# Performance work log

Measured on AMD Instinct MI355X. Metric: run time of the kernel, lower is better.

Reference implementation:

```python
import jax, jax.numpy as jnp
import numpy as np

DIM = 1024
HEADS = 16
HEAD_DIM = DIM // HEADS
SCALE = HEAD_DIM ** -0.5


def setup_inputs() -> dict:
    key = jax.random.key(0)
    ks = jax.random.split(key, 9)
    b, n, m = 4, 1024, 1024
    x = jax.random.normal(ks[0], (b, n, DIM), dtype=jnp.float32)
    context = jax.random.normal(ks[1], (b, m, DIM), dtype=jnp.float32)
    mask = jax.random.randint(ks[2], (b, n, 32, 32), 0, 2, dtype=jnp.int32)
    s = DIM ** -0.5
    Wq = jax.random.normal(ks[3], (DIM, DIM), dtype=jnp.float32) * s
    bq = jnp.zeros((DIM,), dtype=jnp.float32)
    Wkv = jax.random.normal(ks[4], (DIM, 2 * DIM), dtype=jnp.float32) * s
    bkv = jnp.zeros((2 * DIM,), dtype=jnp.float32)
    Wp = jax.random.normal(ks[5], (DIM, DIM), dtype=jnp.float32) * s
    bp = jnp.zeros((DIM,), dtype=jnp.float32)
    return {"x": x, "context": context, "mask": mask,
            "Wq": Wq, "bq": bq, "Wkv": Wkv, "bkv": bkv, "Wp": Wp, "bp": bp}


def reference(x, context, mask, Wq, bq, Wkv, bkv, Wp, bp):
    b, n, _ = x.shape
    m = context.shape[1]
    h, d = HEADS, HEAD_DIM
    # projections
    q = (x @ Wq + bq).reshape(b, n, h, d).transpose(0, 2, 1, 3)       # [b,h,n,d]
    kv = (context @ Wkv + bkv).reshape(b, m, 2, h, d)
    k = kv[:, :, 0].transpose(0, 2, 1, 3)                              # [b,h,m,d]
    v = kv[:, :, 1].transpose(0, 2, 1, 3)                              # [b,h,m,d]
    dots = jnp.einsum('bhnd,bhmd->bhnm', q, k) * SCALE                 # [b,h,n,m]
    # mask: [b,n,H,W] -> [b,1,n,m]; masked_fill where mask == 0
    mflat = mask.reshape(b, n, m)[:, None]                             # [b,1,n,m]
    dots = jnp.where(mflat == 0, -jnp.inf, dots)
    attn = jax.nn.softmax(dots, axis=-1)
    out = jnp.einsum('bhnm,bhmd->bhnd', attn, v)
    out = out.transpose(0, 2, 1, 3).reshape(b, n, h * d)
    return out @ Wp + bp
```

## Files before the change

### kernel.cpp

```cpp
#include <hip/hip_runtime.h>

typedef __bf16 bf16;
typedef __bf16 bf16x8 __attribute__((ext_vector_type(8)));
typedef __bf16 bf16x4 __attribute__((ext_vector_type(4)));
typedef float f32x4 __attribute__((ext_vector_type(4)));
typedef unsigned long long u64;

#define MFMA16(a, b, c) __builtin_amdgcn_mfma_f32_16x16x32_bf16(a, b, c, 0, 0, 0)

__device__ __forceinline__ void gl_lds16(const void* g, void* l) {
  __builtin_amdgcn_global_load_lds(
      (const __attribute__((address_space(1))) unsigned int*)g,
      (__attribute__((address_space(3))) unsigned int*)l, 16, 0, 0);
}

template <int N>
__device__ __forceinline__ void wait_vmcnt() {
  asm volatile("s_waitcnt vmcnt(%0)" ::"n"(N) : "memory");
}

__device__ __forceinline__ void bar() {
  asm volatile("" ::: "memory");
  __builtin_amdgcn_s_barrier();
  asm volatile("" ::: "memory");
}

__global__ __launch_bounds__(256)
void prep_k(const float* __restrict__ Wq, const float* __restrict__ Wkv,
            const float* __restrict__ Wp, const int* __restrict__ mask,
            const float* __restrict__ context, const float* __restrict__ x,
            bf16* __restrict__ BqkvT, bf16* __restrict__ WpT,
            u64* __restrict__ maskbits, bf16* __restrict__ cb,
            bf16* __restrict__ xb) {
  const int bx = blockIdx.x;
  const int tid = threadIdx.x;
  if (bx >= 3328) {
    const size_t i = ((size_t)(bx - 3328) * 256 + tid) * 8;
    f32x4 a0 = *(const f32x4*)(x + i);
    f32x4 a1 = *(const f32x4*)(x + i + 4);
    bf16x8 t;
#pragma unroll
    for (int j = 0; j < 4; ++j) { t[j] = (bf16)a0[j]; t[4 + j] = (bf16)a1[j]; }
    *(bf16x8*)(xb + i) = t;
    return;
  }
  if (bx >= 1280) {
    const size_t i = ((size_t)(bx - 1280) * 256 + tid) * 8;
    f32x4 a0 = *(const f32x4*)(context + i);
    f32x4 a1 = *(const f32x4*)(context + i + 4);
    bf16x8 t;
#pragma unroll
    for (int j = 0; j < 4; ++j) { t[j] = (bf16)a0[j]; t[4 + j] = (bf16)a1[j]; }
    *(bf16x8*)(cb + i) = t;
    return;
  }
  if (bx >= 1024) {
    const int idx = (bx - 1024) * 256 + tid;
    const int4* p = (const int4*)(mask + (size_t)idx * 64);
    u64 v = 0;
#pragma unroll
    for (int i = 0; i < 16; ++i) {
      int4 m = p[i];
      v |= (u64)(m.x != 0) << (4 * i);
      v |= (u64)(m.y != 0) << (4 * i + 1);
      v |= (u64)(m.z != 0) << (4 * i + 2);
      v |= (u64)(m.w != 0) << (4 * i + 3);
    }
    maskbits[idx] = v;
    return;
  }
  const int ct = bx >> 4, rt = bx & 15;
  const float* src;
  bf16* dst;
  int C, c0, drow0;
  if (ct < 16) {
    src = Wq; C = 1024; c0 = ct * 64; dst = BqkvT; drow0 = c0;
  } else if (ct < 48) {
    src = Wkv; C = 2048; c0 = (ct - 16) * 64; dst = BqkvT; drow0 = 1024 + c0;
  } else {
    src = Wp; C = 1024; c0 = (ct - 48) * 64; dst = WpT; drow0 = c0;
  }
  __shared__ bf16 T[64][72];
  const int r0 = rt * 64;
#pragma unroll
  for (int i = 0; i < 2; ++i) {
    int c = i * 256 + tid;
    int row = c >> 3, col = (c & 7) * 8;
    const float* sp = &src[(size_t)(r0 + row) * C + c0 + col];
    f32x4 a0 = *(const f32x4*)sp;
    f32x4 a1 = *(const f32x4*)(sp + 4);
    bf16x8 t;
#pragma unroll
    for (int j = 0; j < 4; ++j) { t[j] = (bf16)a0[j]; t[4 + j] = (bf16)a1[j]; }
    *(bf16x8*)&T[row][col] = t;
  }
  __syncthreads();
#pragma unroll
  for (int i = 0; i < 2; ++i) {
    int c = i * 256 + tid;
    int orow = c >> 3, ocol = (c & 7) * 8;
    bf16x8 v;
#pragma unroll
    for (int j = 0; j < 8; ++j) v[j] = T[ocol + j][orow];
    *(bf16x8*)&dst[(size_t)(drow0 + orow) * 1024 + r0 + ocol] = v;
  }
}

template <int EPI, int BN>
__global__ __launch_bounds__(256, BN == 128 ? 3 : 4)
void gemm_p3(const bf16* __restrict__ A0, const bf16* __restrict__ A1,
             const bf16* __restrict__ Bt, const float* __restrict__ bias0,
             const float* __restrict__ bias1, bf16* __restrict__ oq,
             bf16* __restrict__ ok, bf16* __restrict__ ovt,
             float* __restrict__ outf) {
  constexpr int NJ = BN / 32;
  constexpr int S = 2 + BN / 64;
  __shared__ bf16 As[3][128][32];
  __shared__ bf16 Bs[3][BN][32];
  const int tid = threadIdx.x;
  const int lane = tid & 63;
  const int w = tid >> 6;
  const int wm = (w >> 1) * 64;
  const int wn = (w & 1) * (BN / 2);
  const int l15 = lane & 15, l4 = lane >> 4;
  const int lrow = lane >> 2;
  const int lcg = (lane & 3) ^ ((lrow >> 1) & 3);
  const int rdc = (l4 ^ ((l15 >> 1) & 3)) * 8;
  const int m0 = blockIdx.x * 128;
  const int n0 = blockIdx.y * BN;

  const bf16* Asrc = (EPI == 1) ? ((n0 < 1024) ? A0 : A1) : A0;

  float bc[NJ];
#pragma unroll
  for (int j = 0; j < NJ; ++j) {
    const int col = n0 + wn + j * 16 + l15;
    if (EPI == 1) bc[j] = (col < 1024) ? bias0[col] : bias1[col - 1024];
    else bc[j] = bias0[col];
  }

  f32x4 acc[4][NJ] = {};

#define STAGE(kk, buf)                                                        \
  {                                                                           \
    _Pragma("unroll") for (int it = 0; it < 2; ++it) {                        \
      const int r = w * 32 + it * 16;                                         \
      gl_lds16(&Asrc[(size_t)(m0 + r + lrow) * 1024 + (kk) + lcg * 8],        \
               &As[buf][r][0]);                                               \
    }                                                                         \
    _Pragma("unroll") for (int it = 0; it < BN / 64; ++it) {                  \
      const int r = w * (BN / 4) + it * 16;                                   \
      gl_lds16(&Bt[(size_t)(n0 + r + lrow) * 1024 + (kk) + lcg * 8],          \
               &Bs[buf][r][0]);                                               \
    }                                                                         \
  }

#define COMPUTE(buf)                                                          \
  {                                                                           \
    bf16x8 af[4], bfr[NJ];                                                    \
    _Pragma("unroll") for (int i = 0; i < 4; ++i) af[i] =                     \
        *(const bf16x8*)&As[buf][wm + i * 16 + l15][rdc];                     \
    _Pragma("unroll") for (int j = 0; j < NJ; ++j) bfr[j] =                   \
        *(const bf16x8*)&Bs[buf][wn + j * 16 + l15][rdc];                     \
    _Pragma("unroll") for (int i = 0; i < 4; ++i)                             \
        _Pragma("unroll") for (int j = 0; j < NJ; ++j) acc[i][j] =            \
            MFMA16(af[i], bfr[j], acc[i][j]);                                 \
  }

  STAGE(0, 0);
  STAGE(32, 1);
#pragma unroll 3
  for (int k = 0; k < 30; ++k) {
    wait_vmcnt<S>();
    bar();
    STAGE((k + 2) * 32, (k + 2) % 3);
    COMPUTE(k % 3);
  }
  wait_vmcnt<S>();
  bar();
  COMPUTE(0);
  wait_vmcnt<0>();
  bar();
  COMPUTE(1);
#undef STAGE
#undef COMPUTE

  const float SCALE2 = 0.18033688011112042f;
#pragma unroll
  for (int j = 0; j < NJ; ++j) {
    const int col = n0 + wn + j * 16 + l15;
#pragma unroll
    for (int i = 0; i < 4; ++i) {
#pragma unroll
      for (int r = 0; r < 4; ++r) {
        const int row = m0 + wm + i * 16 + l4 * 4 + r;
        const float v = acc[i][j][r] + bc[j];
        if (EPI == 0) {
          outf[(size_t)row * 1024 + col] = v;
        } else {
          const int b = row >> 10, n = row & 1023;
          if (col < 1024) {
            const int h = col >> 6, d = col & 63;
            oq[(((size_t)(b * 16 + h)) * 1024 + n) * 64 + d] =
                (bf16)(v * SCALE2);
          } else {
            const int ckv = col - 1024;
            const int s = ckv >> 10, c2 = ckv & 1023;
            const int h = c2 >> 6, d = c2 & 63;
            if (s == 0)
              ok[(((size_t)(b * 16 + h)) * 1024 + n) * 64 + d] = (bf16)v;
            else
              ovt[(((size_t)(b * 16 + h)) * 64 + d) * 1024 + n] = (bf16)v;
          }
        }
      }
    }
  }
}

__global__ __launch_bounds__(256, 4)
void attn_kernel(const bf16* __restrict__ q, const bf16* __restrict__ k,
                 const bf16* __restrict__ vT, const u64* __restrict__ maskbits,
                 bf16* __restrict__ ao) {
  const int bh = blockIdx.x;
  const int ntile = blockIdx.y;
  const int b = bh >> 4, h = bh & 15;
  const int tid = threadIdx.x;
  const int lane = tid & 63;
  const int w = tid >> 6;
  const int l15 = lane & 15, l4 = lane >> 4;

  __shared__ bf16 Ks[2][64][64];
  __shared__ bf16 Vts[2][64][64];
  __shared__ bf16 Pw[4][16][64];

  const size_t base = (size_t)bh * 65536;
  const int nrow0 = ntile * 64 + w * 16;

  bf16x8 qf[2];
#pragma unroll
  for (int ks = 0; ks < 2; ++ks)
    qf[ks] = *(const bf16x8*)&q[base + (size_t)(nrow0 + l15) * 64 + ks * 32 +
                                l4 * 8];

  const u64* mb = maskbits + (size_t)(b * 1024 + nrow0 + l15) * 16;

  const int srow = lane >> 3;
  const int sgl = (lane & 7) ^ srow;
  const bf16* kp = &k[base + (size_t)(w * 16 + srow) * 64 + sgl * 8];
  const bf16* vp = &vT[base + (size_t)(w * 16 + srow) * 1024 + sgl * 8];

  const int rc0 = ((0 + l4) ^ (l15 & 7)) * 8;
  const int rc1 = ((4 + l4) ^ (l15 & 7)) * 8;

  f32x4 o[4] = {};
  float lsum = 0.0f;

#define STAGEA(mt_, buf_)                                                     \
  {                                                                           \
    _Pragma("unroll") for (int it = 0; it < 2; ++it) {                        \
      gl_lds16(kp + (size_t)((mt_)*64 + it * 8) * 64,                         \
               &Ks[buf_][w * 16 + it * 8][0]);                                \
      gl_lds16(vp + (size_t)(it * 8) * 1024 + (mt_)*64,                       \
               &Vts[buf_][w * 16 + it * 8][0]);                               \
    }                                                                         \
  }

  STAGEA(0, 0);
  for (int mt = 0; mt < 16; ++mt) {
    const int cur = mt & 1;
    __syncthreads();
    if (mt < 15) STAGEA(mt + 1, cur ^ 1);
    const u64 wmt = mb[mt];

    f32x4 s[4];
#pragma unroll
    for (int sub = 0; sub < 4; ++sub)
      s[sub] = f32x4{-12.f, -12.f, -12.f, -12.f};
    __builtin_amdgcn_s_setprio(1);
#pragma unroll
    for (int sub = 0; sub < 4; ++sub) {
      bf16x8 kf0 = *(const bf16x8*)&Ks[cur][sub * 16 + l15][rc0];
      bf16x8 kf1 = *(const bf16x8*)&Ks[cur][sub * 16 + l15][rc1];
      s[sub] = MFMA16(kf0, qf[0], s[sub]);
      s[sub] = MFMA16(kf1, qf[1], s[sub]);
    }
    __builtin_amdgcn_s_setprio(0);

#pragma unroll
    for (int sub = 0; sub < 4; ++sub) {
      const int kbit = sub * 16 + l4 * 4;
      float p[4];
#pragma unroll
      for (int r = 0; r < 4; ++r) {
        float e = exp2f(s[sub][r]);
        p[r] = ((wmt >> (kbit + r)) & 1) ? e : 0.0f;
      }
      lsum += (p[0] + p[1]) + (p[2] + p[3]);
      bf16x4 pv;
#pragma unroll
      for (int r = 0; r < 4; ++r) pv[r] = (bf16)p[r];
      const int gw = sub * 2 + (l4 >> 1);
      char* pd = (char*)&Pw[w][l15][0] + ((gw ^ (l15 & 7)) * 16 + (l4 & 1) * 8);
      *(bf16x4*)pd = pv;
    }

    bf16x8 af0 = *(const bf16x8*)&Pw[w][l15][rc0];
    bf16x8 af1 = *(const bf16x8*)&Pw[w][l15][rc1];
    __builtin_amdgcn_s_setprio(1);
#pragma unroll
    for (int sub = 0; sub < 4; ++sub) {
      bf16x8 vf0 = *(const bf16x8*)&Vts[cur][sub * 16 + l15][rc0];
      bf16x8 vf1 = *(const bf16x8*)&Vts[cur][sub * 16 + l15][rc1];
      o[sub] = MFMA16(af0, vf0, o[sub]);
      o[sub] = MFMA16(af1, vf1, o[sub]);
    }
    __builtin_amdgcn_s_setprio(0);
  }
#undef STAGEA

  float t = lsum;
  t += __shfl_xor(t, 16);
  t += __shfl_xor(t, 32);
  float inv[4];
#pragma unroll
  for (int r = 0; r < 4; ++r) inv[r] = 1.0f / __shfl(t, l4 * 4 + r);

#pragma unroll
  for (int sub = 0; sub < 4; ++sub) {
#pragma unroll
    for (int r = 0; r < 4; ++r) {
      const int n = nrow0 + l4 * 4 + r;
      const size_t idx =
          ((size_t)(b * 1024 + n)) * 1024 + h * 64 + sub * 16 + l15;
      ao[idx] = (bf16)(o[sub][r] * inv[r]);
    }
  }
}

extern "C" void kernel_launch(void* const* d_in, const int* in_sizes, int n_in,
                              void* d_out, int out_size, void* d_ws,
                              size_t ws_size, hipStream_t stream) {
  const float* x = (const float*)d_in[0];
  const float* context = (const float*)d_in[1];
  const int* mask = (const int*)d_in[2];
  const float* Wq = (const float*)d_in[3];
  const float* bq = (const float*)d_in[4];
  const float* Wkv = (const float*)d_in[5];
  const float* bkv = (const float*)d_in[6];
  const float* Wp = (const float*)d_in[7];
  const float* bp = (const float*)d_in[8];
  float* out = (float*)d_out;

  char* ws = (char*)d_ws;
  bf16* cb = (bf16*)(ws);
  bf16* aow = (bf16*)(ws);
  bf16* xb = (bf16*)(ws + (8ull << 20));
  bf16* BqkvT = (bf16*)(ws + (16ull << 20));
  bf16* qw = (bf16*)(ws + (22ull << 20));
  bf16* kw = (bf16*)(ws + (30ull << 20));
  bf16* vtw = (bf16*)(ws + (38ull << 20));
  u64* maskbits = (u64*)(ws + (46ull << 20));
  bf16* WpT = (bf16*)(ws + (46ull << 20) + (512ull << 10));

  const dim3 blk(256);

  prep_k<<<dim3(5376), blk, 0, stream>>>(Wq, Wkv, Wp, mask, context, x, BqkvT,
                                         WpT, maskbits, cb, xb);

  gemm_p3<1, 128><<<dim3(32, 24), blk, 0, stream>>>(xb, cb, BqkvT, bq, bkv,
                                                    qw, kw, vtw, nullptr);

  attn_kernel<<<dim3(64, 16), blk, 0, stream>>>(qw, kw, vtw, maskbits, aow);

  gemm_p3<0, 64><<<dim3(32, 16), blk, 0, stream>>>(aow, nullptr, WpT, bp,
                                                   nullptr, nullptr, nullptr,
                                                   nullptr, out);
}
```

Baseline: 209.3 us.

## Fuse fp32-to-bf16 activation conversion into QKV projection GEMM

Drops the separate conversion of x and context to bf16 in the prep kernel. A new QKV GEMM kernel reads fp32 activations directly into registers, converts them and writes them to swizzled LDS, while the weights are still staged with global_load_lds in a double-buffered loop. This saves the write and re-read of two 8 MB bf16 intermediates. In exchange the A tile is loaded with fp32 global loads, which doubles its bytes, adds register pressure and conversion work inside the main loop, and the pipeline drops from three stages to two.

Result: slower. 223.3 us (+6.7%).

```diff
diff --git a/kernel.cpp b/kernel.cpp
--- a/kernel.cpp
+++ b/kernel.cpp
@@ -28,32 +28,10 @@
 __global__ __launch_bounds__(256)
 void prep_k(const float* __restrict__ Wq, const float* __restrict__ Wkv,
             const float* __restrict__ Wp, const int* __restrict__ mask,
-            const float* __restrict__ context, const float* __restrict__ x,
             bf16* __restrict__ BqkvT, bf16* __restrict__ WpT,
-            u64* __restrict__ maskbits, bf16* __restrict__ cb,
-            bf16* __restrict__ xb) {
+            u64* __restrict__ maskbits) {
   const int bx = blockIdx.x;
   const int tid = threadIdx.x;
-  if (bx >= 3328) {
-    const size_t i = ((size_t)(bx - 3328) * 256 + tid) * 8;
-    f32x4 a0 = *(const f32x4*)(x + i);
-    f32x4 a1 = *(const f32x4*)(x + i + 4);
-    bf16x8 t;
-#pragma unroll
-    for (int j = 0; j < 4; ++j) { t[j] = (bf16)a0[j]; t[4 + j] = (bf16)a1[j]; }
-    *(bf16x8*)(xb + i) = t;
-    return;
-  }
-  if (bx >= 1280) {
-    const size_t i = ((size_t)(bx - 1280) * 256 + tid) * 8;
-    f32x4 a0 = *(const f32x4*)(context + i);
-    f32x4 a1 = *(const f32x4*)(context + i + 4);
-    bf16x8 t;
-#pragma unroll
-    for (int j = 0; j < 4; ++j) { t[j] = (bf16)a0[j]; t[4 + j] = (bf16)a1[j]; }
-    *(bf16x8*)(cb + i) = t;
-    return;
-  }
   if (bx >= 1024) {
     const int idx = (bx - 1024) * 256 + tid;
     const int4* p = (const int4*)(mask + (size_t)idx * 64);
@@ -103,6 +81,138 @@
 #pragma unroll
     for (int j = 0; j < 8; ++j) v[j] = T[ocol + j][orow];
     *(bf16x8*)&dst[(size_t)(drow0 + orow) * 1024 + r0 + ocol] = v;
+  }
+}
+
+__global__ __launch_bounds__(256, 3)
+void gemm_qkv(const float* __restrict__ x, const float* __restrict__ ctx,
+              const bf16* __restrict__ Bt, const float* __restrict__ bq,
+              const float* __restrict__ bkv, bf16* __restrict__ oq,
+              bf16* __restrict__ ok, bf16* __restrict__ ovt) {
+  __shared__ bf16 As[2][128][32];
+  __shared__ bf16 Bs[2][128][32];
+  const int tid = threadIdx.x;
+  const int lane = tid & 63;
+  const int w = tid >> 6;
+  const int wm = (w >> 1) * 64;
+  const int wn = (w & 1) * 64;
+  const int l15 = lane & 15, l4 = lane >> 4;
+  const int lrow = lane >> 2;
+  const int lcg = (lane & 3) ^ ((lrow >> 1) & 3);
+  const int rdc = (l4 ^ ((l15 >> 1) & 3)) * 8;
+  const int ar = tid >> 1;
+  const int ag = (tid & 1) * 2;
+  const int asw = (ar >> 1) & 3;
+  const int m0 = blockIdx.x * 128;
+  const int n0 = blockIdx.y * 128;
+
+  const float* Af = (n0 < 1024) ? x : ctx;
+
+  float bc[4];
+#pragma unroll
+  for (int j = 0; j < 4; ++j) {
+    const int col = n0 + wn + j * 16 + l15;
+    bc[j] = (col < 1024) ? bq[col] : bkv[col - 1024];
+  }
+
+  f32x4 acc[4][4] = {};
+  f32x4 pf[4];
+  bf16x8 cfA[4], cfB[4], nfA[4], nfB[4];
+
+#define LOADA(kk)                                                             \
+  {                                                                           \
+    const float* ap = &Af[(size_t)(m0 + ar) * 1024 + (kk) + ag * 8];          \
+    pf[0] = *(const f32x4*)ap;                                                \
+    pf[1] = *(const f32x4*)(ap + 4);                                          \
+    pf[2] = *(const f32x4*)(ap + 8);                                          \
+    pf[3] = *(const f32x4*)(ap + 12);                                         \
+  }
+#define COMMITA(buf)                                                          \
+  {                                                                           \
+    bf16x8 t0, t1;                                                            \
+    _Pragma("unroll") for (int u = 0; u < 4; ++u) {                           \
+      t0[u] = (bf16)pf[0][u]; t0[4 + u] = (bf16)pf[1][u];                     \
+      t1[u] = (bf16)pf[2][u]; t1[4 + u] = (bf16)pf[3][u];                     \
+    }                                                                         \
+    *(bf16x8*)&As[buf][ar][(ag ^ asw) * 8] = t0;                              \
+    *(bf16x8*)&As[buf][ar][((ag + 1) ^ asw) * 8] = t1;                        \
+  }
+#define STAGEB(kk, buf)                                                       \
+  _Pragma("unroll") for (int it = 0; it < 2; ++it) {                          \
+    const int r = w * 32 + it * 16;                                           \
+    gl_lds16(&Bt[(size_t)(n0 + r + lrow) * 1024 + (kk) + lcg * 8],            \
+             &Bs[buf][r][0]);                                                 \
+  }
+#define LOADFRAG(dA, dB, buf)                                                 \
+  {                                                                           \
+    _Pragma("unroll") for (int i = 0; i < 4; ++i) dA[i] =                     \
+        *(const bf16x8*)&As[buf][wm + i * 16 + l15][rdc];                     \
+    _Pragma("unroll") for (int j = 0; j < 4; ++j) dB[j] =                     \
+        *(const bf16x8*)&Bs[buf][wn + j * 16 + l15][rdc];                     \
+  }
+#define MFMA_BLK(fA, fB)                                                      \
+  _Pragma("unroll") for (int i = 0; i < 4; ++i)                               \
+      _Pragma("unroll") for (int j = 0; j < 4; ++j) acc[i][j] =               \
+          MFMA16(fA[i], fB[j], acc[i][j]);
+
+  LOADA(0);
+  STAGEB(0, 0);
+  COMMITA(0);
+  __syncthreads();
+  LOADA(32);
+  STAGEB(32, 1);
+  LOADFRAG(cfA, cfB, 0);
+  COMMITA(1);
+
+  for (int t = 0; t < 30; t += 2) {
+    __syncthreads();
+    LOADA((t + 2) * 32);
+    STAGEB((t + 2) * 32, 0);
+    LOADFRAG(nfA, nfB, 1);
+    MFMA_BLK(cfA, cfB);
+    COMMITA(0);
+    __syncthreads();
+    LOADA((t + 3) * 32);
+    STAGEB((t + 3) * 32, 1);
+    LOADFRAG(cfA, cfB, 0);
+    MFMA_BLK(nfA, nfB);
+    COMMITA(1);
+  }
+  __syncthreads();
+  LOADFRAG(nfA, nfB, 1);
+  MFMA_BLK(cfA, cfB);
+  MFMA_BLK(nfA, nfB);
+#undef LOADA
+#undef COMMITA
+#undef STAGEB
+#undef LOADFRAG
+#undef MFMA_BLK
+
+  const float SCALE2 = 0.18033688011112042f;
+#pragma unroll
+  for (int j = 0; j < 4; ++j) {
+    const int col = n0 + wn + j * 16 + l15;
+#pragma unroll
+    for (int i = 0; i < 4; ++i) {
+#pragma unroll
+      for (int r = 0; r < 4; ++r) {
+        const int row = m0 + wm + i * 16 + l4 * 4 + r;
+        const float v = acc[i][j][r] + bc[j];
+        const int b = row >> 10, n = row & 1023;
+        if (col < 1024) {
+          const int h = col >> 6, d = col & 63;
+          oq[(((size_t)(b * 16 + h)) * 1024 + n) * 64 + d] = (bf16)(v * SCALE2);
+        } else {
+          const int ckv = col - 1024;
+          const int s = ckv >> 10, c2 = ckv & 1023;
+          const int h = c2 >> 6, d = c2 & 63;
+          if (s == 0)
+            ok[(((size_t)(b * 16 + h)) * 1024 + n) * 64 + d] = (bf16)v;
+          else
+            ovt[(((size_t)(b * 16 + h)) * 64 + d) * 1024 + n] = (bf16)v;
+        }
+      }
+    }
   }
 }
 
@@ -353,23 +463,21 @@
   float* out = (float*)d_out;
 
   char* ws = (char*)d_ws;
-  bf16* cb = (bf16*)(ws);
   bf16* aow = (bf16*)(ws);
-  bf16* xb = (bf16*)(ws + (8ull << 20));
-  bf16* BqkvT = (bf16*)(ws + (16ull << 20));
-  bf16* qw = (bf16*)(ws + (22ull << 20));
-  bf16* kw = (bf16*)(ws + (30ull << 20));
-  bf16* vtw = (bf16*)(ws + (38ull << 20));
-  u64* maskbits = (u64*)(ws + (46ull << 20));
-  bf16* WpT = (bf16*)(ws + (46ull << 20) + (512ull << 10));
+  bf16* BqkvT = (bf16*)(ws + (8ull << 20));
+  bf16* qw = (bf16*)(ws + (14ull << 20));
+  bf16* kw = (bf16*)(ws + (22ull << 20));
+  bf16* vtw = (bf16*)(ws + (30ull << 20));
+  u64* maskbits = (u64*)(ws + (38ull << 20));
+  bf16* WpT = (bf16*)(ws + (38ull << 20) + (512ull << 10));
 
   const dim3 blk(256);
 
-  prep_k<<<dim3(5376), blk, 0, stream>>>(Wq, Wkv, Wp, mask, context, x, BqkvT,
-                                         WpT, maskbits, cb, xb);
-
-  gemm_p3<1, 128><<<dim3(32, 24), blk, 0, stream>>>(xb, cb, BqkvT, bq, bkv,
-                                                    qw, kw, vtw, nullptr);
+  prep_k<<<dim3(1280), blk, 0, stream>>>(Wq, Wkv, Wp, mask, BqkvT, WpT,
+                                         maskbits);
+
+  gemm_qkv<<<dim3(32, 24), blk, 0, stream>>>(x, context, BqkvT, bq, bkv, qw,
+                                             kw, vtw);
 
   attn_kernel<<<dim3(64, 16), blk, 0, stream>>>(qw, kw, vtw, maskbits, aow);
 
```

## Double query rows per attention wave and add double-buffered QKV GEMM variant

Applied to the files above, without the earlier changes.

The attention kernel now gives each wave 32 query rows instead of 16, so every K/V tile loaded into LDS serves twice as many MFMAs. The grid shrinks to 8 query tiles per head and launch bounds drop to 2 blocks per SM. The QKV projection switches to a new two-stage double-buffered GEMM that replaces the triple-buffered one. The trade-off is more registers and fewer resident waves per CU in exchange for less LDS staging and fewer barriers per MFMA.

After: 212.9 us. About the same (+1.7%).

```diff
diff --git a/kernel.cpp b/kernel.cpp
--- a/kernel.cpp
+++ b/kernel.cpp
@@ -103,6 +103,106 @@
 #pragma unroll
     for (int j = 0; j < 8; ++j) v[j] = T[ocol + j][orow];
     *(bf16x8*)&dst[(size_t)(drow0 + orow) * 1024 + r0 + ocol] = v;
+  }
+}
+
+template <int EPI, int BN>
+__global__ __launch_bounds__(256, 3)
+void gemm_db2(const bf16* __restrict__ A0, const bf16* __restrict__ A1,
+              const bf16* __restrict__ Bt, const float* __restrict__ bias0,
+              const float* __restrict__ bias1, bf16* __restrict__ oq,
+              bf16* __restrict__ ok, bf16* __restrict__ ovt,
+              float* __restrict__ outf) {
+  constexpr int NJ = BN / 32;
+  __shared__ bf16 As[2][128][32];
+  __shared__ bf16 Bs[2][BN][32];
+  const int tid = threadIdx.x;
+  const int lane = tid & 63;
+  const int w = tid >> 6;
+  const int wm = (w >> 1) * 64;
+  const int wn = (w & 1) * (BN / 2);
+  const int l15 = lane & 15, l4 = lane >> 4;
+  const int lrow = lane >> 2;
+  const int lcg = (lane & 3) ^ ((lrow >> 1) & 3);
+  const int rdc = (l4 ^ ((l15 >> 1) & 3)) * 8;
+  const int m0 = blockIdx.x * 128;
+  const int n0 = blockIdx.y * BN;
+
+  const bf16* Asrc = (EPI == 1) ? ((n0 < 1024) ? A0 : A1) : A0;
+
+  f32x4 acc[4][NJ] = {};
+
+#define STAGE(kk, buf)                                                        \
+  {                                                                           \
+    _Pragma("unroll") for (int it = 0; it < 2; ++it) {                        \
+      const int r = w * 32 + it * 16;                                         \
+      gl_lds16(&Asrc[(size_t)(m0 + r + lrow) * 1024 + (kk) + lcg * 8],        \
+               &As[buf][r][0]);                                               \
+    }                                                                         \
+    _Pragma("unroll") for (int it = 0; it < BN / 64; ++it) {                  \
+      const int r = w * (BN / 4) + it * 16;                                   \
+      gl_lds16(&Bt[(size_t)(n0 + r + lrow) * 1024 + (kk) + lcg * 8],          \
+               &Bs[buf][r][0]);                                               \
+    }                                                                         \
+  }
+
+#define COMPUTE(buf)                                                          \
+  {                                                                           \
+    bf16x8 af[4], bfr[NJ];                                                    \
+    _Pragma("unroll") for (int i = 0; i < 4; ++i) af[i] =                     \
+        *(const bf16x8*)&As[buf][wm + i * 16 + l15][rdc];                     \
+    _Pragma("unroll") for (int j = 0; j < NJ; ++j) bfr[j] =                   \
+        *(const bf16x8*)&Bs[buf][wn + j * 16 + l15][rdc];                     \
+    _Pragma("unroll") for (int i = 0; i < 4; ++i)                             \
+        _Pragma("unroll") for (int j = 0; j < NJ; ++j) acc[i][j] =            \
+            MFMA16(af[i], bfr[j], acc[i][j]);                                 \
+  }
+
+  STAGE(0, 0);
+  for (int k = 0; k < 32; k += 2) {
+    __syncthreads();
+    STAGE((k + 1) * 32, 1);
+    COMPUTE(0);
+    __syncthreads();
+    if (k < 30) STAGE((k + 2) * 32, 0);
+    COMPUTE(1);
+  }
+#undef STAGE
+#undef COMPUTE
+
+  const float SCALE2 = 0.18033688011112042f;
+#pragma unroll
+  for (int j = 0; j < NJ; ++j) {
+    const int col = n0 + wn + j * 16 + l15;
+    float bc;
+    if (EPI == 1) bc = (col < 1024) ? bias0[col] : bias1[col - 1024];
+    else bc = bias0[col];
+#pragma unroll
+    for (int i = 0; i < 4; ++i) {
+#pragma unroll
+      for (int r = 0; r < 4; ++r) {
+        const int row = m0 + wm + i * 16 + l4 * 4 + r;
+        const float v = acc[i][j][r] + bc;
+        if (EPI == 0) {
+          outf[(size_t)row * 1024 + col] = v;
+        } else {
+          const int b = row >> 10, n = row & 1023;
+          if (col < 1024) {
+            const int h = col >> 6, d = col & 63;
+            oq[(((size_t)(b * 16 + h)) * 1024 + n) * 64 + d] =
+                (bf16)(v * SCALE2);
+          } else {
+            const int ckv = col - 1024;
+            const int s = ckv >> 10, c2 = ckv & 1023;
+            const int h = c2 >> 6, d = c2 & 63;
+            if (s == 0)
+              ok[(((size_t)(b * 16 + h)) * 1024 + n) * 64 + d] = (bf16)v;
+            else
+              ovt[(((size_t)(b * 16 + h)) * 64 + d) * 1024 + n] = (bf16)v;
+          }
+        }
+      }
+    }
   }
 }
 
@@ -218,7 +318,7 @@
   }
 }
 
-__global__ __launch_bounds__(256, 4)
+__global__ __launch_bounds__(256, 2)
 void attn_kernel(const bf16* __restrict__ q, const bf16* __restrict__ k,
                  const bf16* __restrict__ vT, const u64* __restrict__ maskbits,
                  bf16* __restrict__ ao) {
@@ -232,16 +332,19 @@
 
   __shared__ bf16 Ks[2][64][64];
   __shared__ bf16 Vts[2][64][64];
-  __shared__ bf16 Pw[4][16][64];
+  __shared__ bf16 Pw[4][32][64];
 
   const size_t base = (size_t)bh * 65536;
-  const int nrow0 = ntile * 64 + w * 16;
-
-  bf16x8 qf[2];
-#pragma unroll
-  for (int ks = 0; ks < 2; ++ks)
-    qf[ks] = *(const bf16x8*)&q[base + (size_t)(nrow0 + l15) * 64 + ks * 32 +
-                                l4 * 8];
+  const int nrow0 = ntile * 128 + w * 32;
+
+  bf16x8 qf[2][2];
+#pragma unroll
+  for (int f = 0; f < 2; ++f)
+#pragma unroll
+    for (int ks = 0; ks < 2; ++ks)
+      qf[f][ks] = *(const bf16x8*)&q[base +
+                                     (size_t)(nrow0 + f * 16 + l15) * 64 +
+                                     ks * 32 + l4 * 8];
 
   const u64* mb = maskbits + (size_t)(b * 1024 + nrow0 + l15) * 16;
 
@@ -253,8 +356,8 @@
   const int rc0 = ((0 + l4) ^ (l15 & 7)) * 8;
   const int rc1 = ((4 + l4) ^ (l15 & 7)) * 8;
 
-  f32x4 o[4] = {};
-  float lsum = 0.0f;
+  f32x4 o[2][4] = {};
+  float lsum[2] = {0.0f, 0.0f};
 
 #define STAGEA(mt_, buf_)                                                     \
   {                                                                           \
@@ -271,69 +374,91 @@
     const int cur = mt & 1;
     __syncthreads();
     if (mt < 15) STAGEA(mt + 1, cur ^ 1);
-    const u64 wmt = mb[mt];
-
-    f32x4 s[4];
-#pragma unroll
-    for (int sub = 0; sub < 4; ++sub)
-      s[sub] = f32x4{-12.f, -12.f, -12.f, -12.f};
+    const u64 wm0 = mb[mt];
+    const u64 wm1 = mb[256 + mt];
+
+    f32x4 s[2][4];
+#pragma unroll
+    for (int f = 0; f < 2; ++f)
+#pragma unroll
+      for (int sub = 0; sub < 4; ++sub)
+        s[f][sub] = f32x4{-12.f, -12.f, -12.f, -12.f};
     __builtin_amdgcn_s_setprio(1);
 #pragma unroll
     for (int sub = 0; sub < 4; ++sub) {
       bf16x8 kf0 = *(const bf16x8*)&Ks[cur][sub * 16 + l15][rc0];
       bf16x8 kf1 = *(const bf16x8*)&Ks[cur][sub * 16 + l15][rc1];
-      s[sub] = MFMA16(kf0, qf[0], s[sub]);
-      s[sub] = MFMA16(kf1, qf[1], s[sub]);
+      s[0][sub] = MFMA16(kf0, qf[0][0], s[0][sub]);
+      s[0][sub] = MFMA16(kf1, qf[0][1], s[0][sub]);
+      s[1][sub] = MFMA16(kf0, qf[1][0], s[1][sub]);
+      s[1][sub] = MFMA16(kf1, qf[1][1], s[1][sub]);
     }
     __builtin_amdgcn_s_setprio(0);
 
 #pragma unroll
-    for (int sub = 0; sub < 4; ++sub) {
-      const int kbit = sub * 16 + l4 * 4;
-      float p[4];
-#pragma unroll
-      for (int r = 0; r < 4; ++r) {
-        float e = exp2f(s[sub][r]);
-        p[r] = ((wmt >> (kbit + r)) & 1) ? e : 0.0f;
+    for (int f = 0; f < 2; ++f) {
+      const u64 wmt = f ? wm1 : wm0;
+#pragma unroll
+      for (int sub = 0; sub < 4; ++sub) {
+        const int kbit = sub * 16 + l4 * 4;
+        float p[4];
+#pragma unroll
+        for (int r = 0; r < 4; ++r) {
+          float e = exp2f(s[f][sub][r]);
+          p[r] = ((wmt >> (kbit + r)) & 1) ? e : 0.0f;
+        }
+        lsum[f] += (p[0] + p[1]) + (p[2] + p[3]);
+        bf16x4 pv;
+#pragma unroll
+        for (int r = 0; r < 4; ++r) pv[r] = (bf16)p[r];
+        const int gw = sub * 2 + (l4 >> 1);
+        char* pd = (char*)&Pw[w][f * 16 + l15][0] +
+                   ((gw ^ (l15 & 7)) * 16 + (l4 & 1) * 8);
+        *(bf16x4*)pd = pv;
       }
-      lsum += (p[0] + p[1]) + (p[2] + p[3]);
-      bf16x4 pv;
-#pragma unroll
-      for (int r = 0; r < 4; ++r) pv[r] = (bf16)p[r];
-      const int gw = sub * 2 + (l4 >> 1);
-      char* pd = (char*)&Pw[w][l15][0] + ((gw ^ (l15 & 7)) * 16 + (l4 & 1) * 8);
-      *(bf16x4*)pd = pv;
-    }
-
-    bf16x8 af0 = *(const bf16x8*)&Pw[w][l15][rc0];
-    bf16x8 af1 = *(const bf16x8*)&Pw[w][l15][rc1];
+    }
+
+    bf16x8 af[2][2];
+#pragma unroll
+    for (int f = 0; f < 2; ++f) {
+      af[f][0] = *(const bf16x8*)&Pw[w][f * 16 + l15][rc0];
+      af[f][1] = *(const bf16x8*)&Pw[w][f * 16 + l15][rc1];
+    }
     __builtin_amdgcn_s_setprio(1);
 #pragma unroll
     for (int sub = 0; sub < 4; ++sub) {
       bf16x8 vf0 = *(const bf16x8*)&Vts[cur][sub * 16 + l15][rc0];
       bf16x8 vf1 = *(const bf16x8*)&Vts[cur][sub * 16 + l15][rc1];
-      o[sub] = MFMA16(af0, vf0, o[sub]);
-      o[sub] = MFMA16(af1, vf1, o[sub]);
+      o[0][sub] = MFMA16(af[0][0], vf0, o[0][sub]);
+      o[0][sub] = MFMA16(af[0][1], vf1, o[0][sub]);
+      o[1][sub] = MFMA16(af[1][0], vf0, o[1][sub]);
+      o[1][sub] = MFMA16(af[1][1], vf1, o[1][sub]);
     }
     __builtin_amdgcn_s_setprio(0);
   }
 #undef STAGEA
 
-  float t = lsum;
-  t += __shfl_xor(t, 16);
-  t += __shfl_xor(t, 32);
-  float inv[4];
-#pragma unroll
-  for (int r = 0; r < 4; ++r) inv[r] = 1.0f / __shfl(t, l4 * 4 + r);
-
-#pragma unroll
-  for (int sub = 0; sub < 4; ++sub) {
-#pragma unroll
-    for (int r = 0; r < 4; ++r) {
-      const int n = nrow0 + l4 * 4 + r;
-      const size_t idx =
-          ((size_t)(b * 1024 + n)) * 1024 + h * 64 + sub * 16 + l15;
-      ao[idx] = (bf16)(o[sub][r] * inv[r]);
+  float inv[2][4];
+#pragma unroll
+  for (int f = 0; f < 2; ++f) {
+    float t = lsum[f];
+    t += __shfl_xor(t, 16);
+    t += __shfl_xor(t, 32);
+#pragma unroll
+    for (int r = 0; r < 4; ++r) inv[f][r] = 1.0f / __shfl(t, l4 * 4 + r);
+  }
+
+#pragma unroll
+  for (int f = 0; f < 2; ++f) {
+#pragma unroll
+    for (int sub = 0; sub < 4; ++sub) {
+#pragma unroll
+      for (int r = 0; r < 4; ++r) {
+        const int n = nrow0 + f * 16 + l4 * 4 + r;
+        const size_t idx =
+            ((size_t)(b * 1024 + n)) * 1024 + h * 64 + sub * 16 + l15;
+        ao[idx] = (bf16)(o[f][sub][r] * inv[f][r]);
+      }
     }
   }
 }
@@ -368,10 +493,10 @@
   prep_k<<<dim3(5376), blk, 0, stream>>>(Wq, Wkv, Wp, mask, context, x, BqkvT,
                                          WpT, maskbits, cb, xb);
 
-  gemm_p3<1, 128><<<dim3(32, 24), blk, 0, stream>>>(xb, cb, BqkvT, bq, bkv,
-                                                    qw, kw, vtw, nullptr);
-
-  attn_kernel<<<dim3(64, 16), blk, 0, stream>>>(qw, kw, vtw, maskbits, aow);
+  gemm_db2<1, 128><<<dim3(32, 24), blk, 0, stream>>>(xb, cb, BqkvT, bq, bkv,
+                                                     qw, kw, vtw, nullptr);
+
+  attn_kernel<<<dim3(64, 8), blk, 0, stream>>>(qw, kw, vtw, maskbits, aow);
 
   gemm_p3<0, 64><<<dim3(32, 16), blk, 0, stream>>>(aow, nullptr, WpT, bp,
                                                    nullptr, nullptr, nullptr,
```

## Process 32 query rows per warp in attention to reuse K/V tiles

Applied to the files above, without the earlier changes.

Each attention warp now computes two 16-row query fragments against the same K and V tiles in LDS, so each block covers 128 query rows and the grid is halved. This doubles the MFMA work per LDS load of K/V and halves total K/V staging traffic. Mask words for the next tile are prefetched one iteration early. The cost is more registers (launch bounds lowered to 2 blocks) and fewer blocks in flight, which may leave CUs underused.

Result: slower. 214.1 us (+2.3%).

```diff
diff --git a/kernel.cpp b/kernel.cpp
--- a/kernel.cpp
+++ b/kernel.cpp
@@ -218,7 +218,7 @@
   }
 }
 
-__global__ __launch_bounds__(256, 4)
+__global__ __launch_bounds__(256, 2)
 void attn_kernel(const bf16* __restrict__ q, const bf16* __restrict__ k,
                  const bf16* __restrict__ vT, const u64* __restrict__ maskbits,
                  bf16* __restrict__ ao) {
@@ -232,16 +232,19 @@
 
   __shared__ bf16 Ks[2][64][64];
   __shared__ bf16 Vts[2][64][64];
-  __shared__ bf16 Pw[4][16][64];
+  __shared__ bf16 Pw[4][32][64];
 
   const size_t base = (size_t)bh * 65536;
-  const int nrow0 = ntile * 64 + w * 16;
-
-  bf16x8 qf[2];
-#pragma unroll
-  for (int ks = 0; ks < 2; ++ks)
-    qf[ks] = *(const bf16x8*)&q[base + (size_t)(nrow0 + l15) * 64 + ks * 32 +
-                                l4 * 8];
+  const int nrow0 = ntile * 128 + w * 32;
+
+  bf16x8 qf[2][2];
+#pragma unroll
+  for (int f = 0; f < 2; ++f)
+#pragma unroll
+    for (int ks = 0; ks < 2; ++ks)
+      qf[f][ks] = *(const bf16x8*)&q[base +
+                                     (size_t)(nrow0 + f * 16 + l15) * 64 +
+                                     ks * 32 + l4 * 8];
 
   const u64* mb = maskbits + (size_t)(b * 1024 + nrow0 + l15) * 16;
 
@@ -253,8 +256,8 @@
   const int rc0 = ((0 + l4) ^ (l15 & 7)) * 8;
   const int rc1 = ((4 + l4) ^ (l15 & 7)) * 8;
 
-  f32x4 o[4] = {};
-  float lsum = 0.0f;
+  f32x4 o[2][4] = {};
+  float lsum[2] = {0.0f, 0.0f};
 
 #define STAGEA(mt_, buf_)                                                     \
   {                                                                           \
@@ -267,73 +270,103 @@
   }
 
   STAGEA(0, 0);
+  u64 wm0 = mb[0];
+  u64 wm1 = mb[256];
   for (int mt = 0; mt < 16; ++mt) {
     const int cur = mt & 1;
     __syncthreads();
     if (mt < 15) STAGEA(mt + 1, cur ^ 1);
-    const u64 wmt = mb[mt];
-
-    f32x4 s[4];
-#pragma unroll
-    for (int sub = 0; sub < 4; ++sub)
-      s[sub] = f32x4{-12.f, -12.f, -12.f, -12.f};
+    u64 nm0 = 0, nm1 = 0;
+    if (mt < 15) {
+      nm0 = mb[mt + 1];
+      nm1 = mb[256 + mt + 1];
+    }
+
+    f32x4 s[2][4];
+#pragma unroll
+    for (int f = 0; f < 2; ++f)
+#pragma unroll
+      for (int sub = 0; sub < 4; ++sub)
+        s[f][sub] = f32x4{-12.f, -12.f, -12.f, -12.f};
     __builtin_amdgcn_s_setprio(1);
 #pragma unroll
     for (int sub = 0; sub < 4; ++sub) {
       bf16x8 kf0 = *(const bf16x8*)&Ks[cur][sub * 16 + l15][rc0];
       bf16x8 kf1 = *(const bf16x8*)&Ks[cur][sub * 16 + l15][rc1];
-      s[sub] = MFMA16(kf0, qf[0], s[sub]);
-      s[sub] = MFMA16(kf1, qf[1], s[sub]);
+      s[0][sub] = MFMA16(kf0, qf[0][0], s[0][sub]);
+      s[0][sub] = MFMA16(kf1, qf[0][1], s[0][sub]);
+      s[1][sub] = MFMA16(kf0, qf[1][0], s[1][sub]);
+      s[1][sub] = MFMA16(kf1, qf[1][1], s[1][sub]);
     }
     __builtin_amdgcn_s_setprio(0);
 
 #pragma unroll
-    for (int sub = 0; sub < 4; ++sub) {
-      const int kbit = sub * 16 + l4 * 4;
-      float p[4];
-#pragma unroll
-      for (int r = 0; r < 4; ++r) {
-        float e = exp2f(s[sub][r]);
-        p[r] = ((wmt >> (kbit + r)) & 1) ? e : 0.0f;
+    for (int f = 0; f < 2; ++f) {
+      const u64 wmt = f ? wm1 : wm0;
+#pragma unroll
+      for (int sub = 0; sub < 4; ++sub) {
+        const int kbit = sub * 16 + l4 * 4;
+        float p[4];
+#pragma unroll
+        for (int r = 0; r < 4; ++r) {
+          float e = exp2f(s[f][sub][r]);
+          p[r] = ((wmt >> (kbit + r)) & 1) ? e : 0.0f;
+        }
+        lsum[f] += (p[0] + p[1]) + (p[2] + p[3]);
+        bf16x4 pv;
+#pragma unroll
+        for (int r = 0; r < 4; ++r) pv[r] = (bf16)p[r];
+        const int gw = sub * 2 + (l4 >> 1);
+        char* pd = (char*)&Pw[w][f * 16 + l15][0] +
+                   ((gw ^ (l15 & 7)) * 16 + (l4 & 1) * 8);
+        *(bf16x4*)pd = pv;
       }
-      lsum += (p[0] + p[1]) + (p[2] + p[3]);
-      bf16x4 pv;
-#pragma unroll
-      for (int r = 0; r < 4; ++r) pv[r] = (bf16)p[r];
-      const int gw = sub * 2 + (l4 >> 1);
-      char* pd = (char*)&Pw[w][l15][0] + ((gw ^ (l15 & 7)) * 16 + (l4 & 1) * 8);
-      *(bf16x4*)pd = pv;
-    }
-
-    bf16x8 af0 = *(const bf16x8*)&Pw[w][l15][rc0];
-    bf16x8 af1 = *(const bf16x8*)&Pw[w][l15][rc1];
+    }
+
+    bf16x8 af[2][2];
+#pragma unroll
+    for (int f = 0; f < 2; ++f) {
+      af[f][0] = *(const bf16x8*)&Pw[w][f * 16 + l15][rc0];
+      af[f][1] = *(const bf16x8*)&Pw[w][f * 16 + l15][rc1];
+    }
     __builtin_amdgcn_s_setprio(1);
 #pragma unroll
     for (int sub = 0; sub < 4; ++sub) {
       bf16x8 vf0 = *(const bf16x8*)&Vts[cur][sub * 16 + l15][rc0];
       bf16x8 vf1 = *(const bf16x8*)&Vts[cur][sub * 16 + l15][rc1];
-      o[sub] = MFMA16(af0, vf0, o[sub]);
-      o[sub] = MFMA16(af1, vf1, o[sub]);
+      o[0][sub] = MFMA16(af[0][0], vf0, o[0][sub]);
+      o[0][sub] = MFMA16(af[0][1], vf1, o[0][sub]);
+      o[1][sub] = MFMA16(af[1][0], vf0, o[1][sub]);
+      o[1][sub] = MFMA16(af[1][1], vf1, o[1][sub]);
     }
     __builtin_amdgcn_s_setprio(0);
+
+    wm0 = nm0;
+    wm1 = nm1;
   }
 #undef STAGEA
 
-  float t = lsum;
-  t += __shfl_xor(t, 16);
-  t += __shfl_xor(t, 32);
-  float inv[4];
-#pragma unroll
-  for (int r = 0; r < 4; ++r) inv[r] = 1.0f / __shfl(t, l4 * 4 + r);
-
-#pragma unroll
-  for (int sub = 0; sub < 4; ++sub) {
-#pragma unroll
-    for (int r = 0; r < 4; ++r) {
-      const int n = nrow0 + l4 * 4 + r;
-      const size_t idx =
-          ((size_t)(b * 1024 + n)) * 1024 + h * 64 + sub * 16 + l15;
-      ao[idx] = (bf16)(o[sub][r] * inv[r]);
+  float inv[2][4];
+#pragma unroll
+  for (int f = 0; f < 2; ++f) {
+    float t = lsum[f];
+    t += __shfl_xor(t, 16);
+    t += __shfl_xor(t, 32);
+#pragma unroll
+    for (int r = 0; r < 4; ++r) inv[f][r] = 1.0f / __shfl(t, l4 * 4 + r);
+  }
+
+#pragma unroll
+  for (int f = 0; f < 2; ++f) {
+#pragma unroll
+    for (int sub = 0; sub < 4; ++sub) {
+#pragma unroll
+      for (int r = 0; r < 4; ++r) {
+        const int n = nrow0 + f * 16 + l4 * 4 + r;
+        const size_t idx =
+            ((size_t)(b * 1024 + n)) * 1024 + h * 64 + sub * 16 + l15;
+        ao[idx] = (bf16)(o[f][sub][r] * inv[f][r]);
+      }
     }
   }
 }
@@ -371,7 +404,7 @@
   gemm_p3<1, 128><<<dim3(32, 24), blk, 0, stream>>>(xb, cb, BqkvT, bq, bkv,
                                                     qw, kw, vtw, nullptr);
 
-  attn_kernel<<<dim3(64, 16), blk, 0, stream>>>(qw, kw, vtw, maskbits, aow);
+  attn_kernel<<<dim3(64, 8), blk, 0, stream>>>(qw, kw, vtw, maskbits, aow);
 
   gemm_p3<0, 64><<<dim3(32, 16), blk, 0, stream>>>(aow, nullptr, WpT, bp,
                                                    nullptr, nullptr, nullptr,
```
